# Kernel tuning notes

Hardware: AMD Instinct MI355X
Metric: run time of the kernel (lower is better)

## Reference

```python
import jax, jax.numpy as jnp
import numpy as np

S = 3072      # total tokens across all images
DIM = 1280    # hidden_size
H = 16        # num_heads
HD = DIM // H # head_dim = 80
NSEG = 6      # number of images (cu_seqlens has NSEG+1 entries)


def _rotate_half(x):
    x1, x2 = jnp.split(x, 2, axis=-1)
    return jnp.concatenate([-x2, x1], axis=-1)


def setup_inputs() -> dict:
    key = jax.random.key(0)
    ks = jax.random.split(key, 12)
    hidden_states = jax.random.normal(ks[0], (S, DIM), jnp.float32)
    # realistic vision rotary embedding: half-dim inv_freq, repeated to head_dim
    inv_freq = 1.0 / (10000.0 ** (jnp.arange(0, HD // 2, dtype=jnp.float32) / (HD // 2)))
    freqs = jnp.arange(S, dtype=jnp.float32)[:, None] * inv_freq[None, :]  # [S, HD/2]
    emb = jnp.concatenate([freqs, freqs], axis=-1)  # [S, HD]
    cos = jnp.cos(emb)
    sin = jnp.sin(emb)
    sc = 0.02
    wq = jax.random.normal(ks[1], (DIM, DIM), jnp.float32) * sc
    bq = jax.random.normal(ks[2], (DIM,), jnp.float32) * sc
    wk = jax.random.normal(ks[3], (DIM, DIM), jnp.float32) * sc
    bk = jax.random.normal(ks[4], (DIM,), jnp.float32) * sc
    wv = jax.random.normal(ks[5], (DIM, DIM), jnp.float32) * sc
    bv = jax.random.normal(ks[6], (DIM,), jnp.float32) * sc
    wo = jax.random.normal(ks[7], (DIM, DIM), jnp.float32) * sc
    bo = jax.random.normal(ks[8], (DIM,), jnp.float32) * sc
    cu_seqlens = (jnp.arange(NSEG + 1, dtype=jnp.int32) * (S // NSEG))  # [0,512,...,3072]
    return dict(hidden_states=hidden_states, cos=cos, sin=sin,
                wq=wq, bq=bq, wk=wk, bk=bk, wv=wv, bv=bv, wo=wo, bo=bo,
                cu_seqlens=cu_seqlens)


def reference(hidden_states, cos, sin, wq, bq, wk, bk, wv, bv, wo, bo, cu_seqlens):
    seq_length = hidden_states.shape[0]
    scaling = HD ** (-0.5)
    # QKV projections (torch Linear: x @ W.T + b)
    q = (hidden_states @ wq.T + bq).reshape(seq_length, H, HD)
    k = (hidden_states @ wk.T + bk).reshape(seq_length, H, HD)
    v = (hidden_states @ wv.T + bv).reshape(seq_length, H, HD)
    # apply_rotary_pos_emb_vision: cos/sin [S, HD] broadcast over head axis
    c = cos[:, None, :]
    s = sin[:, None, :]
    q = q * c + _rotate_half(q) * s
    k = k * c + _rotate_half(k) * s
    # block-diagonal (per-image) attention via segment mask
    seg = jnp.searchsorted(cu_seqlens[1:], jnp.arange(seq_length), side='right')
    mask = seg[:, None] == seg[None, :]  # [S, S] bool
    scores = jnp.einsum('shd,thd->hst', q, k) * scaling  # [H, S, S]
    scores = jnp.where(mask[None, :, :], scores, jnp.finfo(scores.dtype).min)
    attn = jax.nn.softmax(scores, axis=-1)
    out = jnp.einsum('hst,thd->shd', attn, v).reshape(seq_length, DIM)
    return out @ wo.T + bo
```

## Files before the change

kernel.cpp:

```cpp
#include <hip/hip_runtime.h>
#include <hip/hip_bf16.h>
#include <hip/hip_fp16.h>
#include <cstdint>
#include <cstddef>

typedef _Float16 f16;
typedef f16 f16x4 __attribute__((ext_vector_type(4)));
typedef f16 f16x8 __attribute__((ext_vector_type(8)));
typedef float f32x4 __attribute__((ext_vector_type(4)));

#define S_LEN 3072
#define DIM 1280
#define NH 16
#define HD 80
#define SEG 512

#define MFMA16F(a, b, c) __builtin_amdgcn_mfma_f32_16x16x32_f16((a), (b), (c), 0, 0, 0)

__device__ __forceinline__ void gl2lds16(const void* g, void* l) {
    __builtin_amdgcn_global_load_lds(
        (const __attribute__((address_space(1))) unsigned int*)g,
        (__attribute__((address_space(3))) unsigned int*)l, 16, 0, 0);
}

__global__ __launch_bounds__(256) void cvt_kernel(
    const float* __restrict__ hs,
    const float* __restrict__ wq, const float* __restrict__ wk,
    const float* __restrict__ wv, const float* __restrict__ wo,
    f16* __restrict__ hs16,
    f16* __restrict__ wq16, f16* __restrict__ wk16,
    f16* __restrict__ wv16, f16* __restrict__ wo16)
{
    const int m = blockIdx.y;
    const float* src; f16* dst; int n4;
    if (m == 0)      { src = hs; dst = hs16; n4 = S_LEN * DIM / 4; }
    else if (m == 1) { src = wq; dst = wq16; n4 = DIM * DIM / 4; }
    else if (m == 2) { src = wk; dst = wk16; n4 = DIM * DIM / 4; }
    else if (m == 3) { src = wv; dst = wv16; n4 = DIM * DIM / 4; }
    else             { src = wo; dst = wo16; n4 = DIM * DIM / 4; }
    int idx = blockIdx.x * 256 + threadIdx.x;
    if (idx >= n4) return;
    f32x4 v = *(const f32x4*)(src + (size_t)idx * 4);
    f16x4 o;
#pragma unroll
    for (int e = 0; e < 4; ++e) o[e] = (f16)v[e];
    *(f16x4*)(dst + (size_t)idx * 4) = o;
}

__global__ __launch_bounds__(256) void gemm_f16_kernel(
    const f16* __restrict__ A,
    const f16* __restrict__ W0, const f16* __restrict__ W1, const f16* __restrict__ W2,
    const float* __restrict__ b0, const float* __restrict__ b1, const float* __restrict__ b2,
    f16* __restrict__ O0, f16* __restrict__ O1, f16* __restrict__ O2,
    float* __restrict__ OF, int mode_base)
{
    const int mode = mode_base + blockIdx.z;
    const f16* W = (mode == 1) ? W1 : (mode == 2) ? W2 : W0;
    const float* bias = (mode == 1) ? b1 : (mode == 2) ? b2 : b0;

    __shared__ __align__(16) f16 As[128 * 32];
    __shared__ __align__(16) f16 Bs[128 * 32];

    const int tid = threadIdx.x;
    const int lane = tid & 63;
    const int lane15 = tid & 15;
    const int quad = lane >> 4;
    const int w = tid >> 6;
    const int wm = (w >> 1) * 64;
    const int wn = (w & 1) * 64;
    const int m0 = blockIdx.x * 128;
    const int n0 = blockIdx.y * 128;

    const int srow = w * 32 + (lane >> 2);
    const int scol = (lane & 3) * 8;
    const f16* gA0 = A + (size_t)(m0 + srow) * DIM + scol;
    const f16* gA1 = A + (size_t)(m0 + srow + 16) * DIM + scol;
    const f16* gB0 = W + (size_t)(n0 + srow) * DIM + scol;
    const f16* gB1 = W + (size_t)(n0 + srow + 16) * DIM + scol;
    f16* lA0 = As + (w * 32) * 32;
    f16* lA1 = As + (w * 32 + 16) * 32;
    f16* lB0 = Bs + (w * 32) * 32;
    f16* lB1 = Bs + (w * 32 + 16) * 32;

    f32x4 acc[4][4];
#pragma unroll
    for (int i = 0; i < 4; ++i)
#pragma unroll
        for (int j = 0; j < 4; ++j)
            acc[i][j] = (f32x4){0.f, 0.f, 0.f, 0.f};

    for (int kt = 0; kt < DIM / 32; ++kt) {
        __syncthreads();
        gl2lds16(gA0 + kt * 32, lA0);
        gl2lds16(gA1 + kt * 32, lA1);
        gl2lds16(gB0 + kt * 32, lB0);
        gl2lds16(gB1 + kt * 32, lB1);
        __syncthreads();

        f16x8 fa[4], fb[4];
#pragma unroll
        for (int i = 0; i < 4; ++i)
            fa[i] = *(const f16x8*)(As + (wm + i * 16 + lane15) * 32 + quad * 8);
#pragma unroll
        for (int j = 0; j < 4; ++j)
            fb[j] = *(const f16x8*)(Bs + (wn + j * 16 + lane15) * 32 + quad * 8);
#pragma unroll
        for (int i = 0; i < 4; ++i)
#pragma unroll
            for (int j = 0; j < 4; ++j)
                acc[i][j] = MFMA16F(fa[i], fb[j], acc[i][j]);
    }

    float bvv[4];
#pragma unroll
    for (int j = 0; j < 4; ++j)
        bvv[j] = bias[n0 + wn + j * 16 + lane15];

    if (mode == 3) {
#pragma unroll
        for (int i = 0; i < 4; ++i)
#pragma unroll
            for (int j = 0; j < 4; ++j)
#pragma unroll
                for (int r = 0; r < 4; ++r) {
                    int row = m0 + wm + i * 16 + quad * 4 + r;
                    int col = n0 + wn + j * 16 + lane15;
                    OF[(size_t)row * DIM + col] = acc[i][j][r] + bvv[j];
                }
    } else {
        f16* O = (mode == 0) ? O0 : (mode == 1) ? O1 : O2;
#pragma unroll
        for (int i = 0; i < 4; ++i)
#pragma unroll
            for (int j = 0; j < 4; ++j)
#pragma unroll
                for (int r = 0; r < 4; ++r) {
                    int row = m0 + wm + i * 16 + quad * 4 + r;
                    int col = n0 + wn + j * 16 + lane15;
                    O[(size_t)row * DIM + col] = (f16)(acc[i][j][r] + bvv[j]);
                }
    }
}

__global__ __launch_bounds__(256) void rope_kernel(
    f16* __restrict__ qb, f16* __restrict__ kb,
    const float* __restrict__ cosb, const float* __restrict__ sinb)
{
    int idx = blockIdx.x * 256 + threadIdx.x;
    int j = idx % 40;
    int t = idx / 40;
    int h = t % NH; t /= NH;
    int s = t % S_LEN;
    int which = t / S_LEN;
    f16* buf = which ? kb : qb;
    float c  = cosb[s * HD + j];
    float sn = sinb[s * HD + j];
    size_t base = (size_t)s * DIM + h * HD + j;
    float x1 = (float)buf[base];
    float x2 = (float)buf[base + 40];
    buf[base]      = (f16)(x1 * c - x2 * sn);
    buf[base + 40] = (f16)(x2 * c + x1 * sn);
}

__global__ __launch_bounds__(256) void attn_kernel(
    const f16* __restrict__ q, const f16* __restrict__ k,
    const f16* __restrict__ v, f16* __restrict__ o)
{
    const int h = blockIdx.x;
    const int g = blockIdx.y;
    const int qc = blockIdx.z;
    const int tid = threadIdx.x;
    const int lane15 = tid & 15;
    const int quad = (tid & 63) >> 4;
    const int w = tid >> 6;
    const int qbase = g * SEG + qc * 64;
    const float scaling = 0.11180339887498948f;

    __shared__ __align__(16) f16 Ks[64 * 88];
    __shared__ __align__(16) f16 Vt[80 * 72];
    __shared__ __align__(16) f16 Ps[4][16 * 72];

    f16x8 zf;
#pragma unroll
    for (int e = 0; e < 8; ++e) zf[e] = (f16)0.0f;

    f16x8 fq[3];
    const int sq = qbase + w * 16 + lane15;
#pragma unroll
    for (int kc = 0; kc < 3; ++kc) {
        if (kc == 2 && quad >= 2) fq[kc] = zf;
        else fq[kc] = *(const f16x8*)(q + (size_t)sq * DIM + h * HD + kc * 32 + quad * 8);
    }

    float m_run[4], l_run[4];
    f32x4 Oa[5];
#pragma unroll
    for (int r = 0; r < 4; ++r) { m_run[r] = -1e30f; l_run[r] = 0.f; }
#pragma unroll
    for (int nt = 0; nt < 5; ++nt) Oa[nt] = (f32x4){0.f, 0.f, 0.f, 0.f};

    for (int kt = 0; kt < 8; ++kt) {
        __syncthreads();
        const int kb = g * SEG + kt * 64;
#pragma unroll
        for (int c = tid; c < 1280; c += 256) {
            int mat = c >= 640;
            int cc = c - mat * 640;
            int r = cc / 10;
            int c8 = (cc - r * 10) * 8;
            if (!mat) {
                *(f16x8*)(Ks + r * 88 + c8) =
                    *(const f16x8*)(k + (size_t)(kb + r) * DIM + h * HD + c8);
            } else {
                f16x8 vv = *(const f16x8*)(v + (size_t)(kb + r) * DIM + h * HD + c8);
#pragma unroll
                for (int e = 0; e < 8; ++e) Vt[(c8 + e) * 72 + r] = vv[e];
            }
        }
        __syncthreads();

        f32x4 sa[4];
#pragma unroll
        for (int nt = 0; nt < 4; ++nt) sa[nt] = (f32x4){0.f, 0.f, 0.f, 0.f};
#pragma unroll
        for (int kc = 0; kc < 3; ++kc) {
#pragma unroll
            for (int nt = 0; nt < 4; ++nt) {
                f16x8 fk;
                if (kc == 2 && quad >= 2) fk = zf;
                else fk = *(const f16x8*)(Ks + (nt * 16 + lane15) * 88 + kc * 32 + quad * 8);
                sa[nt] = MFMA16F(fq[kc], fk, sa[nt]);
            }
        }

        float mt[4];
#pragma unroll
        for (int r = 0; r < 4; ++r) mt[r] = -1e30f;
#pragma unroll
        for (int nt = 0; nt < 4; ++nt)
#pragma unroll
            for (int r = 0; r < 4; ++r) {
                float s = sa[nt][r] * scaling;
                sa[nt][r] = s;
                mt[r] = fmaxf(mt[r], s);
            }
#pragma unroll
        for (int off = 1; off < 16; off <<= 1)
#pragma unroll
            for (int r = 0; r < 4; ++r)
                mt[r] = fmaxf(mt[r], __shfl_xor(mt[r], off, 64));

        float alpha[4], lt[4];
#pragma unroll
        for (int r = 0; r < 4; ++r) {
            float mn = fmaxf(m_run[r], mt[r]);
            alpha[r] = __expf(m_run[r] - mn);
            m_run[r] = mn;
            lt[r] = 0.f;
        }
#pragma unroll
        for (int nt = 0; nt < 4; ++nt)
#pragma unroll
            for (int r = 0; r < 4; ++r) {
                float p = __expf(sa[nt][r] - m_run[r]);
                sa[nt][r] = p;
                lt[r] += p;
            }
#pragma unroll
        for (int off = 1; off < 16; off <<= 1)
#pragma unroll
            for (int r = 0; r < 4; ++r)
                lt[r] += __shfl_xor(lt[r], off, 64);
#pragma unroll
        for (int r = 0; r < 4; ++r) l_run[r] = l_run[r] * alpha[r] + lt[r];

#pragma unroll
        for (int nt = 0; nt < 4; ++nt)
#pragma unroll
            for (int r = 0; r < 4; ++r)
                Ps[w][(quad * 4 + r) * 72 + nt * 16 + lane15] = (f16)sa[nt][r];
        __syncthreads();

#pragma unroll
        for (int nt = 0; nt < 5; ++nt)
#pragma unroll
            for (int r = 0; r < 4; ++r) Oa[nt][r] *= alpha[r];
#pragma unroll
        for (int kc2 = 0; kc2 < 2; ++kc2) {
            f16x8 fp = *(const f16x8*)(Ps[w] + lane15 * 72 + kc2 * 32 + quad * 8);
#pragma unroll
            for (int nt = 0; nt < 5; ++nt) {
                f16x8 fv = *(const f16x8*)(Vt + (nt * 16 + lane15) * 72 + kc2 * 32 + quad * 8);
                Oa[nt] = MFMA16F(fp, fv, Oa[nt]);
            }
        }
    }

#pragma unroll
    for (int r = 0; r < 4; ++r) {
        float inv = 1.0f / l_run[r];
        int row = qbase + w * 16 + quad * 4 + r;
#pragma unroll
        for (int nt = 0; nt < 5; ++nt)
            o[(size_t)row * DIM + h * HD + nt * 16 + lane15] = (f16)(Oa[nt][r] * inv);
    }
}

extern "C" void kernel_launch(void* const* d_in, const int* in_sizes, int n_in,
                              void* d_out, int out_size, void* d_ws, size_t ws_size,
                              hipStream_t stream)
{
    const float* hs   = (const float*)d_in[0];
    const float* cosb = (const float*)d_in[1];
    const float* sinb = (const float*)d_in[2];
    const float* wq   = (const float*)d_in[3];
    const float* bq   = (const float*)d_in[4];
    const float* wk   = (const float*)d_in[5];
    const float* bk   = (const float*)d_in[6];
    const float* wv   = (const float*)d_in[7];
    const float* bv   = (const float*)d_in[8];
    const float* wo   = (const float*)d_in[9];
    const float* bo   = (const float*)d_in[10];

    const size_t SD = (size_t)S_LEN * DIM;
    const size_t WW = (size_t)DIM * DIM;
    f16* hs16 = (f16*)d_ws;
    f16* wq16 = hs16 + SD;
    f16* wk16 = wq16 + WW;
    f16* wv16 = wk16 + WW;
    f16* wo16 = wv16 + WW;
    f16* q16  = wo16 + WW;
    f16* k16  = q16 + SD;
    f16* v16  = k16 + SD;
    f16* ao16 = v16 + SD;
    float* outb = (float*)d_out;

    cvt_kernel<<<dim3(S_LEN * DIM / 4 / 256, 5), 256, 0, stream>>>(
        hs, wq, wk, wv, wo, hs16, wq16, wk16, wv16, wo16);
    gemm_f16_kernel<<<dim3(24, 10, 3), 256, 0, stream>>>(
        hs16, wq16, wk16, wv16, bq, bk, bv, q16, k16, v16, nullptr, 0);
    rope_kernel<<<15360, 256, 0, stream>>>(q16, k16, cosb, sinb);
    attn_kernel<<<dim3(NH, 6, 8), 256, 0, stream>>>(q16, k16, v16, ao16);
    gemm_f16_kernel<<<dim3(24, 10, 1), 256, 0, stream>>>(
        ao16, wo16, nullptr, nullptr, bo, nullptr, nullptr,
        nullptr, nullptr, nullptr, outb, 3);
}
```

Measured before the change: 229.5 us.

## Pre-transpose V, vectorize RoPE with folded scale, enlarge attention tiles

```diff
diff --git a/kernel.cpp b/kernel.cpp
--- a/kernel.cpp
+++ b/kernel.cpp
@@ -142,29 +142,72 @@
     }
 }
 
+__global__ __launch_bounds__(256) void vtrans_kernel(
+    const f16* __restrict__ v, f16* __restrict__ vT)
+{
+    const int h = blockIdx.x;
+    const int s0 = blockIdx.y * 128;
+    __shared__ __align__(16) f16 Ls[128 * 128];
+    const int tid = threadIdx.x;
+#pragma unroll
+    for (int c = tid; c < 1280; c += 256) {
+        int r = c / 10;
+        int ch = c - r * 10;
+        int chs = ch ^ ((r >> 3) & 7);
+        *(f16x8*)(Ls + r * 128 + chs * 8) =
+            *(const f16x8*)(v + (size_t)(s0 + r) * DIM + h * HD + ch * 8);
+    }
+    __syncthreads();
+#pragma unroll
+    for (int c = tid; c < 1280; c += 256) {
+        int d = c >> 4;
+        int sc = c & 15;
+        f16x8 ov;
+#pragma unroll
+        for (int e = 0; e < 8; ++e) {
+            int s = sc * 8 + e;
+            ov[e] = Ls[s * 128 + (((d >> 3) ^ (sc & 7)) * 8) + (d & 7)];
+        }
+        *(f16x8*)(vT + (size_t)(h * HD + d) * S_LEN + s0 + sc * 8) = ov;
+    }
+}
+
 __global__ __launch_bounds__(256) void rope_kernel(
     f16* __restrict__ qb, f16* __restrict__ kb,
     const float* __restrict__ cosb, const float* __restrict__ sinb)
 {
     int idx = blockIdx.x * 256 + threadIdx.x;
-    int j = idx % 40;
-    int t = idx / 40;
-    int h = t % NH; t /= NH;
+    int c = idx % 5;
+    int t = idx / 5;
+    int h = t & 15; t >>= 4;
     int s = t % S_LEN;
     int which = t / S_LEN;
     f16* buf = which ? kb : qb;
-    float c  = cosb[s * HD + j];
-    float sn = sinb[s * HD + j];
+    float scale = which ? 1.0f : 0.11180339887498948f;
+    int j = c * 8;
+    f32x4 ca = *(const f32x4*)(cosb + s * HD + j);
+    f32x4 cb = *(const f32x4*)(cosb + s * HD + j + 4);
+    f32x4 sna = *(const f32x4*)(sinb + s * HD + j);
+    f32x4 snb = *(const f32x4*)(sinb + s * HD + j + 4);
     size_t base = (size_t)s * DIM + h * HD + j;
-    float x1 = (float)buf[base];
-    float x2 = (float)buf[base + 40];
-    buf[base]      = (f16)(x1 * c - x2 * sn);
-    buf[base + 40] = (f16)(x2 * c + x1 * sn);
+    f16x8 x1 = *(f16x8*)(buf + base);
+    f16x8 x2 = *(f16x8*)(buf + base + 40);
+    f16x8 o1, o2;
+#pragma unroll
+    for (int e = 0; e < 8; ++e) {
+        float ce = (e < 4) ? ca[e] : cb[e - 4];
+        float se = (e < 4) ? sna[e] : snb[e - 4];
+        float a = (float)x1[e], b = (float)x2[e];
+        o1[e] = (f16)((a * ce - b * se) * scale);
+        o2[e] = (f16)((b * ce + a * se) * scale);
+    }
+    *(f16x8*)(buf + base) = o1;
+    *(f16x8*)(buf + base + 40) = o2;
 }
 
 __global__ __launch_bounds__(256) void attn_kernel(
     const f16* __restrict__ q, const f16* __restrict__ k,
-    const f16* __restrict__ v, f16* __restrict__ o)
+    const f16* __restrict__ vT, f16* __restrict__ o)
 {
     const int h = blockIdx.x;
     const int g = blockIdx.y;
@@ -173,137 +216,145 @@
     const int lane15 = tid & 15;
     const int quad = (tid & 63) >> 4;
     const int w = tid >> 6;
-    const int qbase = g * SEG + qc * 64;
-    const float scaling = 0.11180339887498948f;
-
-    __shared__ __align__(16) f16 Ks[64 * 88];
-    __shared__ __align__(16) f16 Vt[80 * 72];
-    __shared__ __align__(16) f16 Ps[4][16 * 72];
+    const int qbase = g * SEG + qc * 128;
+
+    __shared__ __align__(16) f16 Ks[128 * 88];
+    __shared__ __align__(16) f16 Vt[80 * 136];
+    __shared__ __align__(16) f16 Ps[4][16 * 136];
 
     f16x8 zf;
 #pragma unroll
     for (int e = 0; e < 8; ++e) zf[e] = (f16)0.0f;
 
-    f16x8 fq[3];
-    const int sq = qbase + w * 16 + lane15;
-#pragma unroll
-    for (int kc = 0; kc < 3; ++kc) {
-        if (kc == 2 && quad >= 2) fq[kc] = zf;
-        else fq[kc] = *(const f16x8*)(q + (size_t)sq * DIM + h * HD + kc * 32 + quad * 8);
-    }
-
-    float m_run[4], l_run[4];
-    f32x4 Oa[5];
-#pragma unroll
-    for (int r = 0; r < 4; ++r) { m_run[r] = -1e30f; l_run[r] = 0.f; }
-#pragma unroll
-    for (int nt = 0; nt < 5; ++nt) Oa[nt] = (f32x4){0.f, 0.f, 0.f, 0.f};
-
-    for (int kt = 0; kt < 8; ++kt) {
+    f16x8 fq[2][3];
+#pragma unroll
+    for (int mt = 0; mt < 2; ++mt) {
+        const int row = qbase + w * 32 + mt * 16 + lane15;
+#pragma unroll
+        for (int kc = 0; kc < 3; ++kc) {
+            if (kc == 2 && quad >= 2) fq[mt][kc] = zf;
+            else fq[mt][kc] = *(const f16x8*)(q + (size_t)row * DIM + h * HD + kc * 32 + quad * 8);
+        }
+    }
+
+    float m_run[2][4], l_run[2][4];
+    f32x4 Oa[2][5];
+#pragma unroll
+    for (int mt = 0; mt < 2; ++mt) {
+#pragma unroll
+        for (int r = 0; r < 4; ++r) { m_run[mt][r] = -1e30f; l_run[mt][r] = 0.f; }
+#pragma unroll
+        for (int nt = 0; nt < 5; ++nt) Oa[mt][nt] = (f32x4){0.f, 0.f, 0.f, 0.f};
+    }
+
+    for (int kt = 0; kt < 4; ++kt) {
         __syncthreads();
-        const int kb = g * SEG + kt * 64;
+        const int kb = g * SEG + kt * 128;
 #pragma unroll
         for (int c = tid; c < 1280; c += 256) {
-            int mat = c >= 640;
-            int cc = c - mat * 640;
-            int r = cc / 10;
-            int c8 = (cc - r * 10) * 8;
-            if (!mat) {
-                *(f16x8*)(Ks + r * 88 + c8) =
-                    *(const f16x8*)(k + (size_t)(kb + r) * DIM + h * HD + c8);
-            } else {
-                f16x8 vv = *(const f16x8*)(v + (size_t)(kb + r) * DIM + h * HD + c8);
-#pragma unroll
-                for (int e = 0; e < 8; ++e) Vt[(c8 + e) * 72 + r] = vv[e];
-            }
+            int r = c / 10;
+            int c8 = (c - r * 10) * 8;
+            *(f16x8*)(Ks + r * 88 + c8) =
+                *(const f16x8*)(k + (size_t)(kb + r) * DIM + h * HD + c8);
+        }
+#pragma unroll
+        for (int c = tid; c < 1280; c += 256) {
+            int d = c >> 4;
+            int sc = (c & 15) * 8;
+            *(f16x8*)(Vt + d * 136 + sc) =
+                *(const f16x8*)(vT + (size_t)(h * HD + d) * S_LEN + kb + sc);
         }
         __syncthreads();
 
-        f32x4 sa[4];
-#pragma unroll
-        for (int nt = 0; nt < 4; ++nt) sa[nt] = (f32x4){0.f, 0.f, 0.f, 0.f};
+        f32x4 sa[2][8];
+#pragma unroll
+        for (int mt = 0; mt < 2; ++mt)
+#pragma unroll
+            for (int nt = 0; nt < 8; ++nt) sa[mt][nt] = (f32x4){0.f, 0.f, 0.f, 0.f};
 #pragma unroll
         for (int kc = 0; kc < 3; ++kc) {
 #pragma unroll
-            for (int nt = 0; nt < 4; ++nt) {
+            for (int nt = 0; nt < 8; ++nt) {
                 f16x8 fk;
                 if (kc == 2 && quad >= 2) fk = zf;
                 else fk = *(const f16x8*)(Ks + (nt * 16 + lane15) * 88 + kc * 32 + quad * 8);
-                sa[nt] = MFMA16F(fq[kc], fk, sa[nt]);
+                sa[0][nt] = MFMA16F(fq[0][kc], fk, sa[0][nt]);
+                sa[1][nt] = MFMA16F(fq[1][kc], fk, sa[1][nt]);
             }
         }
 
-        float mt[4];
-#pragma unroll
-        for (int r = 0; r < 4; ++r) mt[r] = -1e30f;
-#pragma unroll
-        for (int nt = 0; nt < 4; ++nt)
+#pragma unroll
+        for (int mt = 0; mt < 2; ++mt) {
+            float mtv[4];
+#pragma unroll
+            for (int r = 0; r < 4; ++r) mtv[r] = -1e30f;
+#pragma unroll
+            for (int nt = 0; nt < 8; ++nt)
+#pragma unroll
+                for (int r = 0; r < 4; ++r) mtv[r] = fmaxf(mtv[r], sa[mt][nt][r]);
+#pragma unroll
+            for (int off = 1; off < 16; off <<= 1)
+#pragma unroll
+                for (int r = 0; r < 4; ++r)
+                    mtv[r] = fmaxf(mtv[r], __shfl_xor(mtv[r], off, 64));
+
+            float alpha[4], lt[4];
 #pragma unroll
             for (int r = 0; r < 4; ++r) {
-                float s = sa[nt][r] * scaling;
-                sa[nt][r] = s;
-                mt[r] = fmaxf(mt[r], s);
+                float mn = fmaxf(m_run[mt][r], mtv[r]);
+                alpha[r] = __expf(m_run[mt][r] - mn);
+                m_run[mt][r] = mn;
+                lt[r] = 0.f;
             }
 #pragma unroll
-        for (int off = 1; off < 16; off <<= 1)
+            for (int nt = 0; nt < 8; ++nt)
+#pragma unroll
+                for (int r = 0; r < 4; ++r) {
+                    float p = __expf(sa[mt][nt][r] - m_run[mt][r]);
+                    sa[mt][nt][r] = p;
+                    lt[r] += p;
+                }
+#pragma unroll
+            for (int off = 1; off < 16; off <<= 1)
+#pragma unroll
+                for (int r = 0; r < 4; ++r)
+                    lt[r] += __shfl_xor(lt[r], off, 64);
 #pragma unroll
             for (int r = 0; r < 4; ++r)
-                mt[r] = fmaxf(mt[r], __shfl_xor(mt[r], off, 64));
-
-        float alpha[4], lt[4];
+                l_run[mt][r] = l_run[mt][r] * alpha[r] + lt[r];
+
+#pragma unroll
+            for (int nt = 0; nt < 8; ++nt)
+#pragma unroll
+                for (int r = 0; r < 4; ++r)
+                    Ps[w][(quad * 4 + r) * 136 + nt * 16 + lane15] = (f16)sa[mt][nt][r];
+
+#pragma unroll
+            for (int nt = 0; nt < 5; ++nt)
+#pragma unroll
+                for (int r = 0; r < 4; ++r) Oa[mt][nt][r] *= alpha[r];
+#pragma unroll
+            for (int kc2 = 0; kc2 < 4; ++kc2) {
+                f16x8 fp = *(const f16x8*)(Ps[w] + lane15 * 136 + kc2 * 32 + quad * 8);
+#pragma unroll
+                for (int nt = 0; nt < 5; ++nt) {
+                    f16x8 fv = *(const f16x8*)(Vt + (nt * 16 + lane15) * 136 + kc2 * 32 + quad * 8);
+                    Oa[mt][nt] = MFMA16F(fp, fv, Oa[mt][nt]);
+                }
+            }
+        }
+    }
+
+#pragma unroll
+    for (int mt = 0; mt < 2; ++mt)
 #pragma unroll
         for (int r = 0; r < 4; ++r) {
-            float mn = fmaxf(m_run[r], mt[r]);
-            alpha[r] = __expf(m_run[r] - mn);
-            m_run[r] = mn;
-            lt[r] = 0.f;
-        }
-#pragma unroll
-        for (int nt = 0; nt < 4; ++nt)
-#pragma unroll
-            for (int r = 0; r < 4; ++r) {
-                float p = __expf(sa[nt][r] - m_run[r]);
-                sa[nt][r] = p;
-                lt[r] += p;
-            }
-#pragma unroll
-        for (int off = 1; off < 16; off <<= 1)
-#pragma unroll
-            for (int r = 0; r < 4; ++r)
-                lt[r] += __shfl_xor(lt[r], off, 64);
-#pragma unroll
-        for (int r = 0; r < 4; ++r) l_run[r] = l_run[r] * alpha[r] + lt[r];
-
-#pragma unroll
-        for (int nt = 0; nt < 4; ++nt)
-#pragma unroll
-            for (int r = 0; r < 4; ++r)
-                Ps[w][(quad * 4 + r) * 72 + nt * 16 + lane15] = (f16)sa[nt][r];
-        __syncthreads();
-
-#pragma unroll
-        for (int nt = 0; nt < 5; ++nt)
-#pragma unroll
-            for (int r = 0; r < 4; ++r) Oa[nt][r] *= alpha[r];
-#pragma unroll
-        for (int kc2 = 0; kc2 < 2; ++kc2) {
-            f16x8 fp = *(const f16x8*)(Ps[w] + lane15 * 72 + kc2 * 32 + quad * 8);
-#pragma unroll
-            for (int nt = 0; nt < 5; ++nt) {
-                f16x8 fv = *(const f16x8*)(Vt + (nt * 16 + lane15) * 72 + kc2 * 32 + quad * 8);
-                Oa[nt] = MFMA16F(fp, fv, Oa[nt]);
-            }
-        }
-    }
-
-#pragma unroll
-    for (int r = 0; r < 4; ++r) {
-        float inv = 1.0f / l_run[r];
-        int row = qbase + w * 16 + quad * 4 + r;
-#pragma unroll
-        for (int nt = 0; nt < 5; ++nt)
-            o[(size_t)row * DIM + h * HD + nt * 16 + lane15] = (f16)(Oa[nt][r] * inv);
-    }
+            float inv = 1.0f / l_run[mt][r];
+            int row = qbase + w * 32 + mt * 16 + quad * 4 + r;
+#pragma unroll
+            for (int nt = 0; nt < 5; ++nt)
+                o[(size_t)row * DIM + h * HD + nt * 16 + lane15] = (f16)(Oa[mt][nt][r] * inv);
+        }
 }
 
 extern "C" void kernel_launch(void* const* d_in, const int* in_sizes, int n_in,
@@ -333,14 +384,16 @@
     f16* k16  = q16 + SD;
     f16* v16  = k16 + SD;
     f16* ao16 = v16 + SD;
+    f16* vT16 = ao16 + SD;
     float* outb = (float*)d_out;
 
     cvt_kernel<<<dim3(S_LEN * DIM / 4 / 256, 5), 256, 0, stream>>>(
         hs, wq, wk, wv, wo, hs16, wq16, wk16, wv16, wo16);
     gemm_f16_kernel<<<dim3(24, 10, 3), 256, 0, stream>>>(
         hs16, wq16, wk16, wv16, bq, bk, bv, q16, k16, v16, nullptr, 0);
-    rope_kernel<<<15360, 256, 0, stream>>>(q16, k16, cosb, sinb);
-    attn_kernel<<<dim3(NH, 6, 8), 256, 0, stream>>>(q16, k16, v16, ao16);
+    vtrans_kernel<<<dim3(NH, 24), 256, 0, stream>>>(v16, vT16);
+    rope_kernel<<<1920, 256, 0, stream>>>(q16, k16, cosb, sinb);
+    attn_kernel<<<dim3(NH, 6, 4), 256, 0, stream>>>(q16, k16, vT16, ao16);
     gemm_f16_kernel<<<dim3(24, 10, 1), 256, 0, stream>>>(
         ao16, wo16, nullptr, nullptr, bo, nullptr, nullptr,
         nullptr, nullptr, nullptr, outb, 3);
```

Result: slower. 238.1 us (+3.8%).
